# Optimization experiments

Hardware: AMD Instinct MI355X
Metric: run time of the kernel (lower is better)

Reference implementation:

```python
import jax, jax.numpy as jnp
import numpy as np

B, K, S, L, D, A = 16, 128, 64, 2, 256, 500  # batch, beam, stack, layers, hidden, max_actions


def setup_inputs() -> dict:
    key = jax.random.key(0)
    k = jax.random.split(key, 8)
    return {
        "gen_ll": jax.random.normal(k[0], (B, K), jnp.float32),
        "trees": jax.random.normal(k[1], (B, K, S, D), jnp.float32),
        "hiddens": jax.random.normal(k[2], (B, K, S + 1, L, D), jnp.float32),
        "cells": jax.random.normal(k[3], (B, K, S + 1, L, D), jnp.float32),
        "actions": jax.random.randint(k[4], (B, K, A), 0, 100, dtype=jnp.int64)
        if jax.config.jax_enable_x64 else jax.random.randint(k[4], (B, K, A), 0, 100),
        "actions_pos": jax.random.randint(k[5], (B, K), 0, A - 1),
        "pointer": jax.random.randint(k[6], (B, K), 0, S),
        "beam_widths": jax.random.randint(k[7], (B,), 1, K + 1),  # >= 1 active beam per batch
    }


def _gather_beam(x, sort_idx):
    # gather along beam dim (axis=1) with broadcast over trailing dims
    idx = sort_idx.reshape(sort_idx.shape + (1,) * (x.ndim - 2))
    return jnp.take_along_axis(x, idx, axis=1)


def reference(gen_ll, trees, hiddens, cells, actions, actions_pos, pointer, beam_widths):
    # BeamItems.shrink(): mask beams outside active width, sort by score desc,
    # then reorder every parallel tensor (stack + action path) by sort_idx.
    order = jnp.arange(K)
    active = order[None, :] < beam_widths[:, None]                    # [B, K] active_idx_mask
    gen_ll_m = jnp.where(active, gen_ll, -jnp.inf)
    sort_idx = jnp.argsort(-gen_ll_m, axis=1)                          # descending sort
    gen_ll_s = jnp.take_along_axis(gen_ll_m, sort_idx, axis=1)

    trees_s = _gather_beam(trees, sort_idx)                            # stack.sort_by
    hiddens_s = _gather_beam(hiddens, sort_idx)
    cells_s = _gather_beam(cells, sort_idx)
    actions_s = _gather_beam(actions, sort_idx)                        # action_path.sort_by
    actions_pos_s = jnp.take_along_axis(actions_pos, sort_idx, axis=1)
    pointer_s = jnp.take_along_axis(pointer, sort_idx, axis=1)         # stack_state.sort_by

    new_beam_widths = jnp.minimum(beam_widths, K)
    # BeamItems.marginal_probs(): logsumexp over active beams (inactive already -inf)
    marginal = jax.nn.logsumexp(gen_ll_s, axis=1)                      # [B]
    # ActionPath.prev_actions(): gather at actions_pos
    prev_actions = jnp.take_along_axis(actions_s, actions_pos_s[:, :, None], axis=2)[:, :, 0]

    return (gen_ll_s, trees_s, hiddens_s, cells_s, marginal,
            actions_s, actions_pos_s, pointer_s, prev_actions, new_beam_widths)
```

## Files before the change

### kernel.cpp

```cpp
#include <hip/hip_runtime.h>
#include <math.h>
#include <float.h>

#define B 16
#define K 128
#define S 64
#define L 2
#define D 256
#define A 500

#define ROW_TREES (S * D)
#define ROW_HID ((S + 1) * L * D)
#define ROW4_TREES (ROW_TREES / 4)
#define ROW4_HID (ROW_HID / 4)

#define NEG_BIG (-1.0e30f)

#define OFF_GENLL 0
#define OFF_TREES 2048
#define OFF_HID   33556480
#define OFF_CELLS 101713920
#define OFF_MARG  169871360
#define OFF_ACT   169871376
#define OFF_APOS  170895376
#define OFF_PTR   170897424
#define OFF_PREV  170899472
#define OFF_NBW   170901520

__global__ void k_sort(const float* __restrict__ gen_ll,
                       const int* __restrict__ actions,
                       const int* __restrict__ actions_pos,
                       const int* __restrict__ pointer,
                       const int* __restrict__ beam_widths,
                       float* __restrict__ out,
                       int* __restrict__ sort_idx)
{
    const int b = blockIdx.x;
    const int k = threadIdx.x;

    __shared__ float key[K];
    __shared__ int   sidx[K];

    const int w = beam_widths[b];
    const float g = gen_ll[b * K + k];
    const float my = (k < w) ? g : NEG_BIG;
    key[k] = my;
    __syncthreads();

    int rank = 0;
#pragma unroll 16
    for (int i = 0; i < K; ++i) {
        const float ki = key[i];
        rank += (ki > my) || (ki == my && i < k);
    }
    sidx[rank] = k;
    __syncthreads();

    const int j = sidx[k];
    sort_idx[b * K + k] = j;

    out[OFF_GENLL + b * K + k] = key[j];

    const int ap = actions_pos[b * K + j];
    out[OFF_APOS + b * K + k] = (float)ap;
    out[OFF_PTR  + b * K + k] = (float)pointer[b * K + j];
    out[OFF_PREV + b * K + k] = (float)actions[(size_t)(b * K + j) * A + ap];

    if (k == 0) {
        float m = NEG_BIG;
        for (int i = 0; i < K; ++i) m = fmaxf(m, key[i]);
        float s = 0.0f;
        for (int i = 0; i < K; ++i) s += expf(key[i] - m);
        out[OFF_MARG + b] = m + logf(s);
        out[OFF_NBW + b] = (float)(w < K ? w : K);
    }
}

__global__ void k_gather_big(const float4* __restrict__ trees,
                             const float4* __restrict__ hiddens,
                             const float4* __restrict__ cells,
                             const int* __restrict__ sort_idx,
                             float* __restrict__ out)
{
    int row = blockIdx.x;
    const float4* src;
    float4* dst;
    int row4;
    int r;
    if (row < B * K) {
        r = row;
        src = trees;
        dst = (float4*)(out + OFF_TREES);
        row4 = ROW4_TREES;
    } else if (row < 2 * B * K) {
        r = row - B * K;
        src = hiddens;
        dst = (float4*)(out + OFF_HID);
        row4 = ROW4_HID;
    } else {
        r = row - 2 * B * K;
        src = cells;
        dst = (float4*)(out + OFF_CELLS);
        row4 = ROW4_HID;
    }

    const int b = r / K;
    const int j = sort_idx[r];

    const float4* s = src + (size_t)(b * K + j) * row4;
    float4* d = dst + (size_t)r * row4;

    for (int t = threadIdx.x; t < row4; t += blockDim.x)
        d[t] = s[t];
}

__global__ void k_gather_actions(const int* __restrict__ actions,
                                 const int* __restrict__ sort_idx,
                                 float* __restrict__ out)
{
    const int r = blockIdx.x;
    const int b = r / K;
    const int j = sort_idx[r];

    const int* s = actions + (size_t)(b * K + j) * A;
    float* d = out + OFF_ACT + (size_t)r * A;

    for (int t = threadIdx.x; t < A; t += blockDim.x)
        d[t] = (float)s[t];
}

extern "C" void kernel_launch(void* const* d_in, const int* in_sizes, int n_in,
                              void* d_out, int out_size, void* d_ws, size_t ws_size,
                              hipStream_t stream)
{
    const float* gen_ll      = (const float*)d_in[0];
    const float* trees       = (const float*)d_in[1];
    const float* hiddens     = (const float*)d_in[2];
    const float* cells       = (const float*)d_in[3];
    const int*   actions     = (const int*)d_in[4];
    const int*   actions_pos = (const int*)d_in[5];
    const int*   pointer     = (const int*)d_in[6];
    const int*   beam_widths = (const int*)d_in[7];
    float* out = (float*)d_out;
    int* sort_idx = (int*)d_ws;

    k_sort<<<B, K, 0, stream>>>(gen_ll, actions, actions_pos, pointer,
                                beam_widths, out, sort_idx);
    k_gather_big<<<3 * B * K, 256, 0, stream>>>((const float4*)trees,
                                                (const float4*)hiddens,
                                                (const float4*)cells,
                                                sort_idx, out);
    k_gather_actions<<<B * K, 128, 0, stream>>>(actions, sort_idx, out);
}
```

Before: 290.3 us.

## Fuse sort and gathers into one kernel with per-block redundant ranking

```diff
diff --git a/kernel.cpp b/kernel.cpp
--- a/kernel.cpp
+++ b/kernel.cpp
@@ -1,6 +1,5 @@
 #include <hip/hip_runtime.h>
 #include <math.h>
-#include <float.h>
 
 #define B 16
 #define K 128
@@ -9,10 +8,8 @@
 #define D 256
 #define A 500
 
-#define ROW_TREES (S * D)
-#define ROW_HID ((S + 1) * L * D)
-#define ROW4_TREES (ROW_TREES / 4)
-#define ROW4_HID (ROW_HID / 4)
+#define ROW4_TREES 4096
+#define ROW4_HID   8320
 
 #define NEG_BIG (-1.0e30f)
 
@@ -27,106 +24,118 @@
 #define OFF_PREV  170899472
 #define OFF_NBW   170901520
 
-__global__ void k_sort(const float* __restrict__ gen_ll,
-                       const int* __restrict__ actions,
-                       const int* __restrict__ actions_pos,
-                       const int* __restrict__ pointer,
-                       const int* __restrict__ beam_widths,
-                       float* __restrict__ out,
-                       int* __restrict__ sort_idx)
+#define NB_SORT B
+#define NB_ACT  (B * K)
+#define NB_BIG  (3 * B * K)
+#define GRID (NB_SORT + NB_ACT + NB_BIG)
+
+template<int N4>
+__device__ __forceinline__ void copy_row(const float4* __restrict__ s,
+                                         float4* __restrict__ d, int tid)
 {
-    const int b = blockIdx.x;
-    const int k = threadIdx.x;
+    constexpr int FULL = N4 / 256;
+    constexpr int REM  = N4 % 256;
+#pragma unroll 8
+    for (int i = 0; i < FULL; ++i)
+        d[i * 256 + tid] = s[i * 256 + tid];
+    if (REM && tid < REM)
+        d[FULL * 256 + tid] = s[FULL * 256 + tid];
+}
 
+__global__ void __launch_bounds__(256)
+k_fused(const float* __restrict__ gen_ll,
+        const float4* __restrict__ trees,
+        const float4* __restrict__ hiddens,
+        const float4* __restrict__ cells,
+        const int* __restrict__ actions,
+        const int* __restrict__ actions_pos,
+        const int* __restrict__ pointer,
+        const int* __restrict__ beam_widths,
+        float* __restrict__ out)
+{
     __shared__ float key[K];
     __shared__ int   sidx[K];
+    __shared__ float red[4];
+
+    const int tid = threadIdx.x;
+    const int bid = blockIdx.x;
+
+    int type, b, k = 0, r = 0, seg = 0;
+    if (bid < NB_SORT) {
+        type = 0; b = bid;
+    } else if (bid < NB_SORT + NB_ACT) {
+        type = 1; r = bid - NB_SORT; b = r >> 7; k = r & 127;
+    } else {
+        type = 2;
+        const int idx = bid - (NB_SORT + NB_ACT);
+        seg = idx % 3; r = idx / 3; b = r >> 7; k = r & 127;
+    }
 
     const int w = beam_widths[b];
-    const float g = gen_ll[b * K + k];
-    const float my = (k < w) ? g : NEG_BIG;
-    key[k] = my;
+    if (tid < K) key[tid] = (tid < w) ? gen_ll[b * K + tid] : NEG_BIG;
+    __syncthreads();
+    if (tid < K) {
+        const float my = key[tid];
+        int rank = 0;
+#pragma unroll 16
+        for (int i = 0; i < K; ++i) {
+            const float ki = key[i];
+            rank += (ki > my) || (ki == my && i < tid);
+        }
+        sidx[rank] = tid;
+    }
     __syncthreads();
 
-    int rank = 0;
-#pragma unroll 16
-    for (int i = 0; i < K; ++i) {
-        const float ki = key[i];
-        rank += (ki > my) || (ki == my && i < k);
+    if (type == 2) {
+        const int j = sidx[k];
+        if (seg == 0) {
+            copy_row<ROW4_TREES>(trees + (size_t)(b * K + j) * ROW4_TREES,
+                                 (float4*)(out + OFF_TREES) + (size_t)r * ROW4_TREES, tid);
+        } else {
+            const float4* src = (seg == 1) ? hiddens : cells;
+            float* dst0 = out + ((seg == 1) ? OFF_HID : OFF_CELLS);
+            copy_row<ROW4_HID>(src + (size_t)(b * K + j) * ROW4_HID,
+                               (float4*)dst0 + (size_t)r * ROW4_HID, tid);
+        }
+    } else if (type == 1) {
+        const int j = sidx[k];
+        const int* s = actions + (size_t)(b * K + j) * A;
+        float* d = out + OFF_ACT + (size_t)r * A;
+        if (tid < A) d[tid] = (float)s[tid];
+        const int t2 = tid + 256;
+        if (t2 < A) d[t2] = (float)s[t2];
+    } else {
+        if (tid < K) {
+            const int j = sidx[tid];
+            out[OFF_GENLL + b * K + tid] = key[j];
+            const int ap = actions_pos[b * K + j];
+            out[OFF_APOS + b * K + tid] = (float)ap;
+            out[OFF_PTR  + b * K + tid] = (float)pointer[b * K + j];
+            out[OFF_PREV + b * K + tid] = (float)actions[(size_t)(b * K + j) * A + ap];
+        }
+        const float v = (tid < K) ? key[tid] : NEG_BIG;
+        if (tid < 128) {
+            float m = v;
+#pragma unroll
+            for (int mask = 32; mask >= 1; mask >>= 1)
+                m = fmaxf(m, __shfl_xor(m, mask, 64));
+            if ((tid & 63) == 0) red[tid >> 6] = m;
+        }
+        __syncthreads();
+        const float m = fmaxf(red[0], red[1]);
+        if (tid < 128) {
+            float e = expf(v - m);
+#pragma unroll
+            for (int mask = 32; mask >= 1; mask >>= 1)
+                e += __shfl_xor(e, mask, 64);
+            if ((tid & 63) == 0) red[2 + (tid >> 6)] = e;
+        }
+        __syncthreads();
+        if (tid == 0) {
+            out[OFF_MARG + b] = m + logf(red[2] + red[3]);
+            out[OFF_NBW + b] = (float)(w < K ? w : K);
+        }
     }
-    sidx[rank] = k;
-    __syncthreads();
-
-    const int j = sidx[k];
-    sort_idx[b * K + k] = j;
-
-    out[OFF_GENLL + b * K + k] = key[j];
-
-    const int ap = actions_pos[b * K + j];
-    out[OFF_APOS + b * K + k] = (float)ap;
-    out[OFF_PTR  + b * K + k] = (float)pointer[b * K + j];
-    out[OFF_PREV + b * K + k] = (float)actions[(size_t)(b * K + j) * A + ap];
-
-    if (k == 0) {
-        float m = NEG_BIG;
-        for (int i = 0; i < K; ++i) m = fmaxf(m, key[i]);
-        float s = 0.0f;
-        for (int i = 0; i < K; ++i) s += expf(key[i] - m);
-        out[OFF_MARG + b] = m + logf(s);
-        out[OFF_NBW + b] = (float)(w < K ? w : K);
-    }
-}
-
-__global__ void k_gather_big(const float4* __restrict__ trees,
-                             const float4* __restrict__ hiddens,
-                             const float4* __restrict__ cells,
-                             const int* __restrict__ sort_idx,
-                             float* __restrict__ out)
-{
-    int row = blockIdx.x;
-    const float4* src;
-    float4* dst;
-    int row4;
-    int r;
-    if (row < B * K) {
-        r = row;
-        src = trees;
-        dst = (float4*)(out + OFF_TREES);
-        row4 = ROW4_TREES;
-    } else if (row < 2 * B * K) {
-        r = row - B * K;
-        src = hiddens;
-        dst = (float4*)(out + OFF_HID);
-        row4 = ROW4_HID;
-    } else {
-        r = row - 2 * B * K;
-        src = cells;
-        dst = (float4*)(out + OFF_CELLS);
-        row4 = ROW4_HID;
-    }
-
-    const int b = r / K;
-    const int j = sort_idx[r];
-
-    const float4* s = src + (size_t)(b * K + j) * row4;
-    float4* d = dst + (size_t)r * row4;
-
-    for (int t = threadIdx.x; t < row4; t += blockDim.x)
-        d[t] = s[t];
-}
-
-__global__ void k_gather_actions(const int* __restrict__ actions,
-                                 const int* __restrict__ sort_idx,
-                                 float* __restrict__ out)
-{
-    const int r = blockIdx.x;
-    const int b = r / K;
-    const int j = sort_idx[r];
-
-    const int* s = actions + (size_t)(b * K + j) * A;
-    float* d = out + OFF_ACT + (size_t)r * A;
-
-    for (int t = threadIdx.x; t < A; t += blockDim.x)
-        d[t] = (float)s[t];
 }
 
 extern "C" void kernel_launch(void* const* d_in, const int* in_sizes, int n_in,
@@ -142,13 +151,8 @@
     const int*   pointer     = (const int*)d_in[6];
     const int*   beam_widths = (const int*)d_in[7];
     float* out = (float*)d_out;
-    int* sort_idx = (int*)d_ws;
 
-    k_sort<<<B, K, 0, stream>>>(gen_ll, actions, actions_pos, pointer,
-                                beam_widths, out, sort_idx);
-    k_gather_big<<<3 * B * K, 256, 0, stream>>>((const float4*)trees,
-                                                (const float4*)hiddens,
-                                                (const float4*)cells,
-                                                sort_idx, out);
-    k_gather_actions<<<B * K, 128, 0, stream>>>(actions, sort_idx, out);
+    k_fused<<<GRID, 256, 0, stream>>>(gen_ll, (const float4*)trees,
+                                      (const float4*)hiddens, (const float4*)cells,
+                                      actions, actions_pos, pointer, beam_widths, out);
 }
```

Result: faster. 282.6 us (-2.6%).
